# Optimization experiments

Measured on AMD Instinct MI355X. Metric: run time of the kernel, lower is better.

The kernel has to match this reference:

```python
import jax, jax.numpy as jnp
import numpy as np

B, T, IN, H, STEPS = 32768, 11, 2, 64, 80


def gru_cell(x, h, W_ih, W_hh, b_ih, b_hh):
    # PyTorch GRU cell: gates ordered (r, z, n)
    gi = x @ W_ih.T + b_ih            # [B, 3H]
    gh = h @ W_hh.T + b_hh            # [B, 3H]
    gi_r, gi_z, gi_n = jnp.split(gi, 3, axis=-1)
    gh_r, gh_z, gh_n = jnp.split(gh, 3, axis=-1)
    r = jax.nn.sigmoid(gi_r + gh_r)
    z = jax.nn.sigmoid(gi_z + gh_z)
    n = jnp.tanh(gi_n + r * gh_n)
    return (1.0 - z) * n + z * h


def setup_inputs() -> dict:
    key = jax.random.key(0)
    ks = jax.random.split(key, 20)
    s = 1.0 / np.sqrt(H)
    u = lambda k, shape: jax.random.uniform(k, shape, jnp.float32, -s, s)
    inp = {"x": jax.random.normal(ks[0], (B, T, IN), jnp.float32)}
    i = 1
    for pfx, in0 in (("e", IN), ("d", IN)):
        for l, d_in in ((0, in0), (1, H)):
            inp[f"{pfx}W_ih{l}"] = u(ks[i], (3 * H, d_in)); i += 1
            inp[f"{pfx}W_hh{l}"] = u(ks[i], (3 * H, H)); i += 1
            inp[f"{pfx}b_ih{l}"] = u(ks[i], (3 * H,)); i += 1
            inp[f"{pfx}b_hh{l}"] = u(ks[i], (3 * H,)); i += 1
    inp["fc_W"] = u(ks[17], (2, H))
    inp["fc_b"] = u(ks[18], (2,))
    return inp


def reference(x, eW_ih0, eW_hh0, eb_ih0, eb_hh0, eW_ih1, eW_hh1, eb_ih1, eb_hh1,
              dW_ih0, dW_hh0, db_ih0, db_hh0, dW_ih1, dW_hh1, db_ih1, db_hh1,
              fc_W, fc_b):
    b = x.shape[0]
    h0 = jnp.zeros((b, H), x.dtype)
    h1 = jnp.zeros((b, H), x.dtype)

    # ---- encoder: 2-layer GRU over time (dropout inactive in eval) ----
    def enc_step(carry, xt):
        c0, c1 = carry
        c0 = gru_cell(xt, c0, eW_ih0, eW_hh0, eb_ih0, eb_hh0)
        c1 = gru_cell(c0, c1, eW_ih1, eW_hh1, eb_ih1, eb_hh1)
        return (c0, c1), None

    (h0, h1), _ = jax.lax.scan(enc_step, (h0, h1), jnp.swapaxes(x, 0, 1))

    def dec_step(carry, _):
        inp, c0, c1 = carry
        c0 = gru_cell(inp, c0, dW_ih0, dW_hh0, db_ih0, db_hh0)
        c1 = gru_cell(c0, c1, dW_ih1, dW_hh1, db_ih1, db_hh1)
        pred = c1 @ fc_W.T + fc_b     # [B, 2]
        return (pred, c0, c1), pred

    init = (x[:, -1, :], h0, h1)
    _, preds = jax.lax.scan(dec_step, init, None, length=STEPS)  # [80, B, 2]
    return jnp.swapaxes(preds, 0, 1)  # [B, 80, 2]
```

## Files before the change

### kernel.cpp

```cpp
#include <hip/hip_runtime.h>
#include <cstddef>

#define T_SEQ 11
#define STEPS 80

typedef _Float16 f16;
typedef _Float16 f16x4 __attribute__((ext_vector_type(4)));
typedef _Float16 f16x8 __attribute__((ext_vector_type(8)));
typedef float    f32x4 __attribute__((ext_vector_type(4)));

#define SRC (-1.44269504f)
#define SNC ( 2.88539008f)

__device__ __forceinline__ f32x4 mfma16(f16x8 a, f16x8 b, f32x4 c) {
    return __builtin_amdgcn_mfma_f32_16x16x32_f16(a, b, c, 0, 0, 0);
}
__device__ __forceinline__ float exp2r(float x) { return __builtin_amdgcn_exp2f(x); }

__device__ __forceinline__ f16x8 wfrag(const float* __restrict__ W, int row, int k0, float sc) {
    f16x8 r;
    #pragma unroll
    for (int i = 0; i < 8; ++i) r[i] = (f16)(sc * W[row * 64 + k0 + i]);
    return r;
}
__device__ __forceinline__ f16x8 cfrag(const float* __restrict__ Wih0,
                                       const float* __restrict__ fcW, int row, int k0, float sc) {
    f16x8 r;
    #pragma unroll
    for (int i = 0; i < 8; ++i)
        r[i] = (f16)(sc * (Wih0[row * 2] * fcW[k0 + i] + Wih0[row * 2 + 1] * fcW[64 + k0 + i]));
    return r;
}

struct WSet {
    f16x8 xR[2], xZ[2], xN[2];
    f16x8 hR[2], hZ[2], hN[2];
};

__device__ __forceinline__ void load_h_frags(WSet& W, const float* __restrict__ Whh,
                                             int jA, int quad)
{
    #pragma unroll
    for (int ks = 0; ks < 2; ++ks) {
        const int k0 = ks * 32 + quad * 8;
        W.hR[ks] = wfrag(Whh, jA,       k0, SRC);
        W.hZ[ks] = wfrag(Whh, jA + 64,  k0, SRC);
        W.hN[ks] = wfrag(Whh, jA + 128, k0, SNC);
    }
}
__device__ __forceinline__ void load_x_frags(WSet& W, const float* __restrict__ Wx,
                                             int jA, int quad)
{
    #pragma unroll
    for (int ks = 0; ks < 2; ++ks) {
        const int k0 = ks * 32 + quad * 8;
        W.xR[ks] = wfrag(Wx, jA,       k0, SRC);
        W.xZ[ks] = wfrag(Wx, jA + 64,  k0, SRC);
        W.xN[ks] = wfrag(Wx, jA + 128, k0, SNC);
    }
}

template<bool XM, int CT>
__device__ __forceinline__ void cellH(const WSet& W, const float* __restrict__ sb,
    const f16* __restrict__ Xs, const f16* __restrict__ Hs, f16* __restrict__ Dst,
    f16x4& ho, const f32x4* __restrict__ xw, float2 xv,
    int j4, int ro0, int ro1, int wo)
{
    const f32x4 bR  = *(const f32x4*)(sb + CT * 256 +       j4);
    const f32x4 bZ  = *(const f32x4*)(sb + CT * 256 +  64 + j4);
    const f32x4 bNi = *(const f32x4*)(sb + CT * 256 + 128 + j4);
    const f32x4 bNh = *(const f32x4*)(sb + CT * 256 + 192 + j4);
    f16x8 hb0 = *(const f16x8*)(Hs + ro0);
    f16x8 hb1 = *(const f16x8*)(Hs + ro1);
    f32x4 aR  = mfma16(W.hR[0], hb0, bR);
    f32x4 aZ  = mfma16(W.hZ[0], hb0, bZ);
    f32x4 aNh = mfma16(W.hN[0], hb0, bNh);
    aR  = mfma16(W.hR[1], hb1, aR);
    aZ  = mfma16(W.hZ[1], hb1, aZ);
    aNh = mfma16(W.hN[1], hb1, aNh);
    f32x4 aNi;
    if constexpr (XM) {
        f16x8 xb0 = *(const f16x8*)(Xs + ro0);
        f16x8 xb1 = *(const f16x8*)(Xs + ro1);
        aR  = mfma16(W.xR[0], xb0, aR);    aR  = mfma16(W.xR[1], xb1, aR);
        aZ  = mfma16(W.xZ[0], xb0, aZ);    aZ  = mfma16(W.xZ[1], xb1, aZ);
        aNi = mfma16(W.xN[0], xb0, bNi);   aNi = mfma16(W.xN[1], xb1, aNi);
    } else {
        aR  += xv.x * xw[0] + xv.y * xw[1];
        aZ  += xv.x * xw[2] + xv.y * xw[3];
        aNi  = bNi + xv.x * xw[4] + xv.y * xw[5];
    }
    f16x4 o;
    #pragma unroll
    for (int i = 0; i < 4; ++i) {
        const float r = __builtin_amdgcn_rcpf(1.f + exp2r(aR[i]));
        const float z = __builtin_amdgcn_rcpf(1.f + exp2r(aZ[i]));
        const float n = 1.f - 2.f * __builtin_amdgcn_rcpf(1.f + exp2r(aNi[i] + r * aNh[i]));
        const float h = n + z * ((float)ho[i] - n);
        o[i] = (f16)h;
    }
    ho = o;
    *(f16x4*)(Dst + wo) = o;
}

__global__ __launch_bounds__(512, 4)
void gru_traj_pipe1(
    const float* __restrict__ x,
    const float* __restrict__ eWih0, const float* __restrict__ eWhh0,
    const float* __restrict__ ebih0, const float* __restrict__ ebhh0,
    const float* __restrict__ eWih1, const float* __restrict__ eWhh1,
    const float* __restrict__ ebih1, const float* __restrict__ ebhh1,
    const float* __restrict__ dWih0, const float* __restrict__ dWhh0,
    const float* __restrict__ dbih0, const float* __restrict__ dbhh0,
    const float* __restrict__ dWih1, const float* __restrict__ dWhh1,
    const float* __restrict__ dbih1, const float* __restrict__ dbhh1,
    const float* __restrict__ fcW,  const float* __restrict__ fcb,
    float* __restrict__ out)
{
    __shared__ f16 h0b[4][1024];
    __shared__ f16 h1b[4][1024];
    __shared__ float2 xe[T_SEQ * 32];
    __shared__ float sbias[4 * 256];
    __shared__ f16 sfc[1024];
    __shared__ float sfcb[2];

    const int tid  = threadIdx.x;
    const int lane = tid & 63;
    const int wv   = __builtin_amdgcn_readfirstlane(tid >> 6);
    const bool isL0 = wv < 4;
    const int jg   = wv & 3;
    const int quad = lane >> 4;
    const int col  = lane & 15;
    const int r0   = blockIdx.x * 32;

    {
        const float2* x2 = (const float2*)x;
        for (int i = tid; i < 32 * T_SEQ; i += 512) {
            const int row = i / T_SEQ, t = i - row * T_SEQ;
            xe[t * 32 + row] = x2[(size_t)r0 * T_SEQ + i];
        }
    }
    for (int i = tid; i < 2048; i += 512) {
        ((f16*)h0b)[i] = (f16)0.f; ((f16*)h1b)[i] = (f16)0.f;
    }
    if (tid < 64) {
        const int j = tid;
        sbias[       j] = SRC * (ebih0[j] + ebhh0[j]);
        sbias[ 64 + j] = SRC * (ebih0[64 + j] + ebhh0[64 + j]);
        sbias[128 + j] = SNC * ebih0[128 + j];
        sbias[192 + j] = SNC * ebhh0[128 + j];
        sbias[256 +       j] = SRC * (ebih1[j] + ebhh1[j]);
        sbias[256 +  64 + j] = SRC * (ebih1[64 + j] + ebhh1[64 + j]);
        sbias[256 + 128 + j] = SNC * ebih1[128 + j];
        sbias[256 + 192 + j] = SNC * ebhh1[128 + j];
    }
    for (int e = tid; e < 1024; e += 512) {
        const int ks = e >> 9, rr = e & 511;
        const int lne = rr >> 3, ki = rr & 7;
        const int c = lne & 15, q = lne >> 4;
        const int k = ks * 32 + q * 8 + ki;
        sfc[ks * 512 + lne * 8 + ki] = (c < 2) ? (f16)fcW[c * 64 + k] : (f16)0.f;
    }
    if (tid < 2) sfcb[tid] = fcb[tid];

    const int c7  = col & 7;
    const int ro0 = col * 64 + ((quad ^ c7) << 3);
    const int ro1 = col * 64 + (((4 + quad) ^ c7) << 3);
    const int wo  = col * 64 + ((((jg << 1) | (quad >> 1)) ^ c7) << 3) + ((quad & 1) << 2);
    const int jA  = jg * 16 + col;
    const int j4  = jg * 16 + quad * 4;

    f16x4 hoA, hoB;
    #pragma unroll
    for (int i = 0; i < 4; ++i) { hoA[i] = (f16)0.f; hoB[i] = (f16)0.f; }

    WSet W;
    f32x4 xw[6];
    if (isL0) {
        load_h_frags(W, eWhh0, jA, quad);
        #pragma unroll
        for (int rg = 0; rg < 4; ++rg) {
            xw[0][rg] = SRC * eWih0[(j4 + rg) * 2];        xw[1][rg] = SRC * eWih0[(j4 + rg) * 2 + 1];
            xw[2][rg] = SRC * eWih0[(64 + j4 + rg) * 2];   xw[3][rg] = SRC * eWih0[(64 + j4 + rg) * 2 + 1];
            xw[4][rg] = SNC * eWih0[(128 + j4 + rg) * 2];  xw[5][rg] = SNC * eWih0[(128 + j4 + rg) * 2 + 1];
        }
    } else {
        load_h_frags(W, eWhh1, jA, quad);
        load_x_frags(W, eWih1, jA, quad);
    }
    __syncthreads();

    #pragma unroll 1
    for (int t = 0; t < T_SEQ; ++t) {
        const int pr = t & 1, pw = pr ^ 1;
        if (isL0) {
            const float2 xv = xe[t * 32 + col];
            cellH<false, 0>(W, sbias, nullptr, h0b[pr * 2 + 0], h0b[pw * 2 + 0], hoA, xw, xv, j4, ro0, ro1, wo);
        } else if (t > 0) {
            cellH<true, 1>(W, sbias, h0b[pr * 2 + 1], h1b[pw * 2 + 1], h1b[pr * 2 + 1], hoB, xw, make_float2(0.f, 0.f), j4, ro0, ro1, wo);
        }
        __syncthreads();
        if (isL0) {
            const float2 xv = xe[t * 32 + 16 + col];
            cellH<false, 0>(W, sbias, nullptr, h0b[pr * 2 + 1], h0b[pw * 2 + 1], hoB, xw, xv, j4, ro0, ro1, wo);
        } else {
            cellH<true, 1>(W, sbias, h0b[pw * 2 + 0], h1b[pr * 2 + 0], h1b[pw * 2 + 0], hoA, xw, make_float2(0.f, 0.f), j4, ro0, ro1, wo);
        }
        __syncthreads();
    }
    if (!isL0)
        cellH<true, 1>(W, sbias, h0b[1 * 2 + 1], h1b[0 * 2 + 1], h1b[1 * 2 + 1], hoB, xw, make_float2(0.f, 0.f), j4, ro0, ro1, wo);
    __syncthreads();

    if (isL0) {
        load_h_frags(W, dWhh0, jA, quad);
        #pragma unroll
        for (int ks = 0; ks < 2; ++ks) {
            const int k0 = ks * 32 + quad * 8;
            W.xR[ks] = cfrag(dWih0, fcW, jA,       k0, SRC);
            W.xZ[ks] = cfrag(dWih0, fcW, jA + 64,  k0, SRC);
            W.xN[ks] = cfrag(dWih0, fcW, jA + 128, k0, SNC);
        }
        #pragma unroll
        for (int rg = 0; rg < 4; ++rg) {
            xw[0][rg] = SRC * dWih0[(j4 + rg) * 2];        xw[1][rg] = SRC * dWih0[(j4 + rg) * 2 + 1];
            xw[2][rg] = SRC * dWih0[(64 + j4 + rg) * 2];   xw[3][rg] = SRC * dWih0[(64 + j4 + rg) * 2 + 1];
            xw[4][rg] = SNC * dWih0[(128 + j4 + rg) * 2];  xw[5][rg] = SNC * dWih0[(128 + j4 + rg) * 2 + 1];
        }
    } else {
        load_h_frags(W, dWhh1, jA, quad);
        load_x_frags(W, dWih1, jA, quad);
    }
    if (tid < 64) {
        const int j = tid;
        const float f0 = fcb[0], f1 = fcb[1];
        sbias[512 +       j] = SRC * (dbih0[j] + dbhh0[j] + dWih0[j * 2] * f0 + dWih0[j * 2 + 1] * f1);
        sbias[512 +  64 + j] = SRC * (dbih0[64 + j] + dbhh0[64 + j] + dWih0[(64 + j) * 2] * f0 + dWih0[(64 + j) * 2 + 1] * f1);
        sbias[512 + 128 + j] = SNC * (dbih0[128 + j] + dWih0[(128 + j) * 2] * f0 + dWih0[(128 + j) * 2 + 1] * f1);
        sbias[512 + 192 + j] = SNC * dbhh0[128 + j];
        sbias[768 +       j] = SRC * (dbih1[j] + dbhh1[j]);
        sbias[768 +  64 + j] = SRC * (dbih1[64 + j] + dbhh1[64 + j]);
        sbias[768 + 128 + j] = SNC * dbih1[128 + j];
        sbias[768 + 192 + j] = SNC * dbhh1[128 + j];
    }
    __syncthreads();

    float* op = out + (size_t)(r0 + jg * 16 + col) * (STEPS * 2);
    auto FCOUT = [&](const f16* __restrict__ h1c) {
        f32x4 pb;
        pb[0] = (quad == 0) ? sfcb[0] : 0.f;
        pb[1] = (quad == 0) ? sfcb[1] : 0.f;
        pb[2] = 0.f; pb[3] = 0.f;
        f16x8 fc0 = *(const f16x8*)(sfc + lane * 8);
        f16x8 fc1 = *(const f16x8*)(sfc + 512 + lane * 8);
        f16x8 hb0 = *(const f16x8*)(h1c + ro0);
        f16x8 hb1 = *(const f16x8*)(h1c + ro1);
        f32x4 p = mfma16(fc0, hb0, pb);
        p = mfma16(fc1, hb1, p);
        if (quad == 0) *(float2*)op = make_float2(p[0], p[1]);
        op += 2;
    };

    if (isL0) {
        const float2 xv = xe[10 * 32 + col];
        cellH<false, 2>(W, sbias, nullptr, h0b[1 * 2 + 0], h0b[0 * 2 + 0], hoA, xw, xv, j4, ro0, ro1, wo);
    }
    __syncthreads();
    if (isL0) {
        const float2 xv = xe[10 * 32 + 16 + col];
        cellH<false, 2>(W, sbias, nullptr, h0b[1 * 2 + 1], h0b[0 * 2 + 1], hoB, xw, xv, j4, ro0, ro1, wo);
    } else {
        cellH<true, 3>(W, sbias, h0b[0 * 2 + 0], h1b[1 * 2 + 0], h1b[0 * 2 + 0], hoA, xw, make_float2(0.f, 0.f), j4, ro0, ro1, wo);
    }
    __syncthreads();

    #pragma unroll 1
    for (int s = 1; s < STEPS; ++s) {
        const int pr = s & 1, pw = pr ^ 1;
        if (isL0) {
            cellH<true, 2>(W, sbias, h1b[pw * 2 + 0], h0b[pw * 2 + 0], h0b[pr * 2 + 0], hoA, xw, make_float2(0.f, 0.f), j4, ro0, ro1, wo);
        } else {
            cellH<true, 3>(W, sbias, h0b[pw * 2 + 1], h1b[pr * 2 + 1], h1b[pw * 2 + 1], hoB, xw, make_float2(0.f, 0.f), j4, ro0, ro1, wo);
            if (jg == 0) FCOUT(h1b[pw * 2 + 0]);
        }
        __syncthreads();
        if (isL0) {
            cellH<true, 2>(W, sbias, h1b[pw * 2 + 1], h0b[pw * 2 + 1], h0b[pr * 2 + 1], hoB, xw, make_float2(0.f, 0.f), j4, ro0, ro1, wo);
        } else {
            cellH<true, 3>(W, sbias, h0b[pr * 2 + 0], h1b[pw * 2 + 0], h1b[pr * 2 + 0], hoA, xw, make_float2(0.f, 0.f), j4, ro0, ro1, wo);
            if (jg == 1) FCOUT(h1b[pw * 2 + 1]);
        }
        __syncthreads();
    }
    if (!isL0) {
        cellH<true, 3>(W, sbias, h0b[1 * 2 + 1], h1b[0 * 2 + 1], h1b[1 * 2 + 1], hoB, xw, make_float2(0.f, 0.f), j4, ro0, ro1, wo);
        if (jg == 0) FCOUT(h1b[1 * 2 + 0]);
    }
    __syncthreads();
    if (!isL0 && jg == 1) FCOUT(h1b[1 * 2 + 1]);
}

extern "C" void kernel_launch(void* const* d_in, const int* in_sizes, int n_in,
                              void* d_out, int out_size, void* d_ws, size_t ws_size,
                              hipStream_t stream) {
    (void)n_in; (void)out_size; (void)d_ws; (void)ws_size;

    const float* x     = (const float*)d_in[0];
    const float* eWih0 = (const float*)d_in[1];
    const float* eWhh0 = (const float*)d_in[2];
    const float* ebih0 = (const float*)d_in[3];
    const float* ebhh0 = (const float*)d_in[4];
    const float* eWih1 = (const float*)d_in[5];
    const float* eWhh1 = (const float*)d_in[6];
    const float* ebih1 = (const float*)d_in[7];
    const float* ebhh1 = (const float*)d_in[8];
    const float* dWih0 = (const float*)d_in[9];
    const float* dWhh0 = (const float*)d_in[10];
    const float* dbih0 = (const float*)d_in[11];
    const float* dbhh0 = (const float*)d_in[12];
    const float* dWih1 = (const float*)d_in[13];
    const float* dWhh1 = (const float*)d_in[14];
    const float* dbih1 = (const float*)d_in[15];
    const float* dbhh1 = (const float*)d_in[16];
    const float* fcW   = (const float*)d_in[17];
    const float* fcb   = (const float*)d_in[18];
    float* out = (float*)d_out;

    const int b = in_sizes[0] / (T_SEQ * 2);
    dim3 grid(b / 32), block(512);
    hipLaunchKernelGGL(gru_traj_pipe1, grid, block, 0, stream,
        x, eWih0, eWhh0, ebih0, ebhh0, eWih1, eWhh1, ebih1, ebhh1,
        dWih0, dWhh0, dbih0, dbhh0, dWih1, dWhh1, dbih1, dbhh1,
        fcW, fcb, out);
}
```

Baseline: 470.0 us.

## Switch GRU kernel to 32x32x16 MFMA tiles with bias folded into MFMA

Replaces the 16x16x32 MFMA cell with a 32x32x16 variant. Each block now handles 64 batch rows with 4 waves instead of 32 rows with 8 waves, so each wave owns a 32-unit half of the hidden dimension. Biases and the 2-wide layer-0 input projection are folded into an extra MFMA by packing weights and a split hi/lo bias into spare K slots, which removes the shared bias table and the scalar FMA path. Wave roles alternate by block parity to balance which SIMD hosts layer 0. This cuts per-wave instruction overhead, but it raises register pressure (larger weight fragments and accumulators) and lowers the wave count per block.

Measured after the change: 485.7 us. 3.3% more time.

```diff
diff --git a/kernel.cpp b/kernel.cpp
--- a/kernel.cpp
+++ b/kernel.cpp
@@ -8,103 +8,87 @@
 typedef _Float16 f16x4 __attribute__((ext_vector_type(4)));
 typedef _Float16 f16x8 __attribute__((ext_vector_type(8)));
 typedef float    f32x4 __attribute__((ext_vector_type(4)));
+typedef float    f32x16 __attribute__((ext_vector_type(16)));
 
 #define SRC (-1.44269504f)
 #define SNC ( 2.88539008f)
 
-__device__ __forceinline__ f32x4 mfma16(f16x8 a, f16x8 b, f32x4 c) {
-    return __builtin_amdgcn_mfma_f32_16x16x32_f16(a, b, c, 0, 0, 0);
+__device__ __forceinline__ f32x16 mfma32(f16x8 a, f16x8 b, f32x16 c) {
+    return __builtin_amdgcn_mfma_f32_32x32x16_f16(a, b, c, 0, 0, 0);
 }
 __device__ __forceinline__ float exp2r(float x) { return __builtin_amdgcn_exp2f(x); }
 
-__device__ __forceinline__ f16x8 wfrag(const float* __restrict__ W, int row, int k0, float sc) {
+__device__ __forceinline__ f16x8 afrag32(const float* __restrict__ W, int rowBase,
+                                         int b31, int hi, int f, float sc) {
     f16x8 r;
+    const int row = rowBase + b31, k0 = f * 16 + hi * 8;
     #pragma unroll
     for (int i = 0; i < 8; ++i) r[i] = (f16)(sc * W[row * 64 + k0 + i]);
     return r;
 }
-__device__ __forceinline__ f16x8 cfrag(const float* __restrict__ Wih0,
-                                       const float* __restrict__ fcW, int row, int k0, float sc) {
+__device__ __forceinline__ f16x8 cfrag32(const float* __restrict__ Wih0,
+                                         const float* __restrict__ fcW, int rowBase,
+                                         int b31, int hi, int f, float sc) {
     f16x8 r;
+    const int row = rowBase + b31, k0 = f * 16 + hi * 8;
     #pragma unroll
     for (int i = 0; i < 8; ++i)
         r[i] = (f16)(sc * (Wih0[row * 2] * fcW[k0 + i] + Wih0[row * 2 + 1] * fcW[64 + k0 + i]));
     return r;
 }
-
-struct WSet {
-    f16x8 xR[2], xZ[2], xN[2];
-    f16x8 hR[2], hZ[2], hN[2];
-};
-
-__device__ __forceinline__ void load_h_frags(WSet& W, const float* __restrict__ Whh,
-                                             int jA, int quad)
+__device__ __forceinline__ f16x8 ex_make(float w0, float w1, float b, int hi) {
+    f16x8 r;
+    #pragma unroll
+    for (int i = 0; i < 8; ++i) r[i] = (f16)0.f;
+    if (hi == 0) {
+        r[0] = (f16)w0; r[1] = (f16)w1;
+        const float bh = (float)(f16)b;
+        r[6] = (f16)bh; r[7] = (f16)(256.f * (b - bh));
+    }
+    return r;
+}
+
+template<bool XM>
+__device__ __forceinline__ void cell32(
+    const f16x8 (&Wh)[3][4], const f16x8 (&Wx)[3][4], const f16x8 (&ex)[4], f16x8 exB,
+    const f16* __restrict__ Xs, const f16* __restrict__ Hs, f16* __restrict__ Dst,
+    f16x4 (&ho)[4], const int (&rd)[4], const int (&wr)[4])
 {
-    #pragma unroll
-    for (int ks = 0; ks < 2; ++ks) {
-        const int k0 = ks * 32 + quad * 8;
-        W.hR[ks] = wfrag(Whh, jA,       k0, SRC);
-        W.hZ[ks] = wfrag(Whh, jA + 64,  k0, SRC);
-        W.hN[ks] = wfrag(Whh, jA + 128, k0, SNC);
-    }
-}
-__device__ __forceinline__ void load_x_frags(WSet& W, const float* __restrict__ Wx,
-                                             int jA, int quad)
-{
-    #pragma unroll
-    for (int ks = 0; ks < 2; ++ks) {
-        const int k0 = ks * 32 + quad * 8;
-        W.xR[ks] = wfrag(Wx, jA,       k0, SRC);
-        W.xZ[ks] = wfrag(Wx, jA + 64,  k0, SRC);
-        W.xN[ks] = wfrag(Wx, jA + 128, k0, SNC);
-    }
-}
-
-template<bool XM, int CT>
-__device__ __forceinline__ void cellH(const WSet& W, const float* __restrict__ sb,
-    const f16* __restrict__ Xs, const f16* __restrict__ Hs, f16* __restrict__ Dst,
-    f16x4& ho, const f32x4* __restrict__ xw, float2 xv,
-    int j4, int ro0, int ro1, int wo)
-{
-    const f32x4 bR  = *(const f32x4*)(sb + CT * 256 +       j4);
-    const f32x4 bZ  = *(const f32x4*)(sb + CT * 256 +  64 + j4);
-    const f32x4 bNi = *(const f32x4*)(sb + CT * 256 + 128 + j4);
-    const f32x4 bNh = *(const f32x4*)(sb + CT * 256 + 192 + j4);
-    f16x8 hb0 = *(const f16x8*)(Hs + ro0);
-    f16x8 hb1 = *(const f16x8*)(Hs + ro1);
-    f32x4 aR  = mfma16(W.hR[0], hb0, bR);
-    f32x4 aZ  = mfma16(W.hZ[0], hb0, bZ);
-    f32x4 aNh = mfma16(W.hN[0], hb0, bNh);
-    aR  = mfma16(W.hR[1], hb1, aR);
-    aZ  = mfma16(W.hZ[1], hb1, aZ);
-    aNh = mfma16(W.hN[1], hb1, aNh);
-    f32x4 aNi;
-    if constexpr (XM) {
-        f16x8 xb0 = *(const f16x8*)(Xs + ro0);
-        f16x8 xb1 = *(const f16x8*)(Xs + ro1);
-        aR  = mfma16(W.xR[0], xb0, aR);    aR  = mfma16(W.xR[1], xb1, aR);
-        aZ  = mfma16(W.xZ[0], xb0, aZ);    aZ  = mfma16(W.xZ[1], xb1, aZ);
-        aNi = mfma16(W.xN[0], xb0, bNi);   aNi = mfma16(W.xN[1], xb1, aNi);
-    } else {
-        aR  += xv.x * xw[0] + xv.y * xw[1];
-        aZ  += xv.x * xw[2] + xv.y * xw[3];
-        aNi  = bNi + xv.x * xw[4] + xv.y * xw[5];
-    }
-    f16x4 o;
-    #pragma unroll
-    for (int i = 0; i < 4; ++i) {
-        const float r = __builtin_amdgcn_rcpf(1.f + exp2r(aR[i]));
-        const float z = __builtin_amdgcn_rcpf(1.f + exp2r(aZ[i]));
-        const float n = 1.f - 2.f * __builtin_amdgcn_rcpf(1.f + exp2r(aNi[i] + r * aNh[i]));
-        const float h = n + z * ((float)ho[i] - n);
-        o[i] = (f16)h;
-    }
-    ho = o;
-    *(f16x4*)(Dst + wo) = o;
-}
-
-__global__ __launch_bounds__(512, 4)
-void gru_traj_pipe1(
+    f32x16 z;
+    #pragma unroll
+    for (int i = 0; i < 16; ++i) z[i] = 0.f;
+    f32x16 aR  = mfma32(ex[0], exB, z);
+    f32x16 aZ  = mfma32(ex[1], exB, z);
+    f32x16 aNi = mfma32(ex[2], exB, z);
+    f32x16 aNh = mfma32(ex[3], exB, z);
+    #pragma unroll
+    for (int f = 0; f < 4; ++f) {
+        const f16x8 hb = *(const f16x8*)(Hs + rd[f]);
+        aR  = mfma32(Wh[0][f], hb, aR);
+        aZ  = mfma32(Wh[1][f], hb, aZ);
+        aNh = mfma32(Wh[2][f], hb, aNh);
+        if constexpr (XM) {
+            const f16x8 xb = *(const f16x8*)(Xs + rd[f]);
+            aR  = mfma32(Wx[0][f], xb, aR);
+            aZ  = mfma32(Wx[1][f], xb, aZ);
+            aNi = mfma32(Wx[2][f], xb, aNi);
+        }
+    }
+    f16x4 o[4];
+    #pragma unroll
+    for (int r = 0; r < 16; ++r) {
+        const float rr = __builtin_amdgcn_rcpf(1.f + exp2r(aR[r]));
+        const float zz = __builtin_amdgcn_rcpf(1.f + exp2r(aZ[r]));
+        const float n  = 1.f - 2.f * __builtin_amdgcn_rcpf(1.f + exp2r(aNi[r] + rr * aNh[r]));
+        const float h  = n + zz * ((float)ho[r >> 2][r & 3] - n);
+        o[r >> 2][r & 3] = (f16)h;
+    }
+    #pragma unroll
+    for (int g = 0; g < 4; ++g) { ho[g] = o[g]; *(f16x4*)(Dst + wr[g]) = o[g]; }
+}
+
+__global__ __launch_bounds__(256, 2)
+void gru_traj_w32(
     const float* __restrict__ x,
     const float* __restrict__ eWih0, const float* __restrict__ eWhh0,
     const float* __restrict__ ebih0, const float* __restrict__ ebhh0,
@@ -117,76 +101,83 @@
     const float* __restrict__ fcW,  const float* __restrict__ fcb,
     float* __restrict__ out)
 {
-    __shared__ f16 h0b[4][1024];
-    __shared__ f16 h1b[4][1024];
-    __shared__ float2 xe[T_SEQ * 32];
-    __shared__ float sbias[4 * 256];
-    __shared__ f16 sfc[1024];
-    __shared__ float sfcb[2];
+    __shared__ f16 h0s[2 * 2 * 2048];
+    __shared__ f16 h1s[2 * 2 * 2048];
+    __shared__ float2 xs[T_SEQ * 64];
+#define H0(p, hf) (h0s + ((p) * 2 + (hf)) * 2048)
+#define H1(p, hf) (h1s + ((p) * 2 + (hf)) * 2048)
 
     const int tid  = threadIdx.x;
     const int lane = tid & 63;
     const int wv   = __builtin_amdgcn_readfirstlane(tid >> 6);
-    const bool isL0 = wv < 4;
-    const int jg   = wv & 3;
-    const int quad = lane >> 4;
-    const int col  = lane & 15;
-    const int r0   = blockIdx.x * 32;
+    const int wvr  = (wv + ((blockIdx.x & 1) << 1)) & 3;
+    const bool isL0 = wvr < 2;
+    const int jh   = wvr & 1;
+    const int b31  = lane & 31;
+    const int hi   = lane >> 5;
+    const int b7   = b31 & 7;
+    const int r0   = blockIdx.x * 64;
 
     {
         const float2* x2 = (const float2*)x;
-        for (int i = tid; i < 32 * T_SEQ; i += 512) {
+        for (int i = tid; i < 64 * T_SEQ; i += 256) {
             const int row = i / T_SEQ, t = i - row * T_SEQ;
-            xe[t * 32 + row] = x2[(size_t)r0 * T_SEQ + i];
-        }
-    }
-    for (int i = tid; i < 2048; i += 512) {
-        ((f16*)h0b)[i] = (f16)0.f; ((f16*)h1b)[i] = (f16)0.f;
-    }
-    if (tid < 64) {
-        const int j = tid;
-        sbias[       j] = SRC * (ebih0[j] + ebhh0[j]);
-        sbias[ 64 + j] = SRC * (ebih0[64 + j] + ebhh0[64 + j]);
-        sbias[128 + j] = SNC * ebih0[128 + j];
-        sbias[192 + j] = SNC * ebhh0[128 + j];
-        sbias[256 +       j] = SRC * (ebih1[j] + ebhh1[j]);
-        sbias[256 +  64 + j] = SRC * (ebih1[64 + j] + ebhh1[64 + j]);
-        sbias[256 + 128 + j] = SNC * ebih1[128 + j];
-        sbias[256 + 192 + j] = SNC * ebhh1[128 + j];
-    }
-    for (int e = tid; e < 1024; e += 512) {
-        const int ks = e >> 9, rr = e & 511;
-        const int lne = rr >> 3, ki = rr & 7;
-        const int c = lne & 15, q = lne >> 4;
-        const int k = ks * 32 + q * 8 + ki;
-        sfc[ks * 512 + lne * 8 + ki] = (c < 2) ? (f16)fcW[c * 64 + k] : (f16)0.f;
-    }
-    if (tid < 2) sfcb[tid] = fcb[tid];
-
-    const int c7  = col & 7;
-    const int ro0 = col * 64 + ((quad ^ c7) << 3);
-    const int ro1 = col * 64 + (((4 + quad) ^ c7) << 3);
-    const int wo  = col * 64 + ((((jg << 1) | (quad >> 1)) ^ c7) << 3) + ((quad & 1) << 2);
-    const int jA  = jg * 16 + col;
-    const int j4  = jg * 16 + quad * 4;
-
-    f16x4 hoA, hoB;
-    #pragma unroll
-    for (int i = 0; i < 4; ++i) { hoA[i] = (f16)0.f; hoB[i] = (f16)0.f; }
-
-    WSet W;
-    f32x4 xw[6];
+            xs[t * 64 + row] = x2[(size_t)r0 * T_SEQ + i];
+        }
+    }
+    for (int i = tid; i < 4096; i += 256) { h0s[i] = (f16)0.f; h1s[i] = (f16)0.f; }
+
+    int rd[4], wr[4];
+    #pragma unroll
+    for (int f = 0; f < 4; ++f) rd[f] = b31 * 64 + (((f * 2 + hi) ^ b7) << 3);
+    #pragma unroll
+    for (int g = 0; g < 4; ++g) wr[g] = b31 * 64 + ((((jh << 2) + g) ^ b7) << 3) + (hi << 2);
+
+    const int jA = jh * 32 + b31;
+
+    f16x8 exB1;
+    #pragma unroll
+    for (int i = 0; i < 8; ++i) exB1[i] = (f16)0.f;
+    if (hi == 0) { exB1[6] = (f16)1.f; exB1[7] = (f16)(1.f / 256.f); }
+    auto exBx = [&](float2 xv) {
+        f16x8 r;
+        #pragma unroll
+        for (int i = 0; i < 8; ++i) r[i] = (f16)0.f;
+        if (hi == 0) { r[0] = (f16)xv.x; r[1] = (f16)xv.y; r[6] = (f16)1.f; r[7] = (f16)(1.f / 256.f); }
+        return r;
+    };
+
+    f16x4 hoA[4], hoB[4];
+    #pragma unroll
+    for (int g = 0; g < 4; ++g) {
+        #pragma unroll
+        for (int i = 0; i < 4; ++i) { hoA[g][i] = (f16)0.f; hoB[g][i] = (f16)0.f; }
+    }
+
+    f16x8 Wh[3][4], Wx[3][4], ex[4];
     if (isL0) {
-        load_h_frags(W, eWhh0, jA, quad);
-        #pragma unroll
-        for (int rg = 0; rg < 4; ++rg) {
-            xw[0][rg] = SRC * eWih0[(j4 + rg) * 2];        xw[1][rg] = SRC * eWih0[(j4 + rg) * 2 + 1];
-            xw[2][rg] = SRC * eWih0[(64 + j4 + rg) * 2];   xw[3][rg] = SRC * eWih0[(64 + j4 + rg) * 2 + 1];
-            xw[4][rg] = SNC * eWih0[(128 + j4 + rg) * 2];  xw[5][rg] = SNC * eWih0[(128 + j4 + rg) * 2 + 1];
-        }
+        #pragma unroll
+        for (int g = 0; g < 3; ++g)
+            #pragma unroll
+            for (int f = 0; f < 4; ++f)
+                Wh[g][f] = afrag32(eWhh0, g * 64 + jh * 32, b31, hi, f, g == 2 ? SNC : SRC);
+        ex[0] = ex_make(SRC * eWih0[jA * 2],         SRC * eWih0[jA * 2 + 1],         SRC * (ebih0[jA] + ebhh0[jA]), hi);
+        ex[1] = ex_make(SRC * eWih0[(64 + jA) * 2],  SRC * eWih0[(64 + jA) * 2 + 1],  SRC * (ebih0[64 + jA] + ebhh0[64 + jA]), hi);
+        ex[2] = ex_make(SNC * eWih0[(128 + jA) * 2], SNC * eWih0[(128 + jA) * 2 + 1], SNC * ebih0[128 + jA], hi);
+        ex[3] = ex_make(0.f, 0.f, SNC * ebhh0[128 + jA], hi);
     } else {
-        load_h_frags(W, eWhh1, jA, quad);
-        load_x_frags(W, eWih1, jA, quad);
+        #pragma unroll
+        for (int g = 0; g < 3; ++g)
+            #pragma unroll
+            for (int f = 0; f < 4; ++f) {
+                const float sc = g == 2 ? SNC : SRC;
+                Wh[g][f] = afrag32(eWhh1, g * 64 + jh * 32, b31, hi, f, sc);
+                Wx[g][f] = afrag32(eWih1, g * 64 + jh * 32, b31, hi, f, sc);
+            }
+        ex[0] = ex_make(0.f, 0.f, SRC * (ebih1[jA] + ebhh1[jA]), hi);
+        ex[1] = ex_make(0.f, 0.f, SRC * (ebih1[64 + jA] + ebhh1[64 + jA]), hi);
+        ex[2] = ex_make(0.f, 0.f, SNC * ebih1[128 + jA], hi);
+        ex[3] = ex_make(0.f, 0.f, SNC * ebhh1[128 + jA], hi);
     }
     __syncthreads();
 
@@ -194,110 +185,128 @@
     for (int t = 0; t < T_SEQ; ++t) {
         const int pr = t & 1, pw = pr ^ 1;
         if (isL0) {
-            const float2 xv = xe[t * 32 + col];
-            cellH<false, 0>(W, sbias, nullptr, h0b[pr * 2 + 0], h0b[pw * 2 + 0], hoA, xw, xv, j4, ro0, ro1, wo);
+            cell32<false>(Wh, Wh, ex, exBx(xs[t * 64 + b31]),
+                          nullptr, H0(pr, 0), H0(pw, 0), hoA, rd, wr);
         } else if (t > 0) {
-            cellH<true, 1>(W, sbias, h0b[pr * 2 + 1], h1b[pw * 2 + 1], h1b[pr * 2 + 1], hoB, xw, make_float2(0.f, 0.f), j4, ro0, ro1, wo);
+            cell32<true>(Wh, Wx, ex, exB1, H0(pr, 1), H1(pw, 1), H1(pr, 1), hoB, rd, wr);
         }
         __syncthreads();
         if (isL0) {
-            const float2 xv = xe[t * 32 + 16 + col];
-            cellH<false, 0>(W, sbias, nullptr, h0b[pr * 2 + 1], h0b[pw * 2 + 1], hoB, xw, xv, j4, ro0, ro1, wo);
+            cell32<false>(Wh, Wh, ex, exBx(xs[t * 64 + 32 + b31]),
+                          nullptr, H0(pr, 1), H0(pw, 1), hoB, rd, wr);
         } else {
-            cellH<true, 1>(W, sbias, h0b[pw * 2 + 0], h1b[pr * 2 + 0], h1b[pw * 2 + 0], hoA, xw, make_float2(0.f, 0.f), j4, ro0, ro1, wo);
+            cell32<true>(Wh, Wx, ex, exB1, H0(pw, 0), H1(pr, 0), H1(pw, 0), hoA, rd, wr);
         }
         __syncthreads();
     }
     if (!isL0)
-        cellH<true, 1>(W, sbias, h0b[1 * 2 + 1], h1b[0 * 2 + 1], h1b[1 * 2 + 1], hoB, xw, make_float2(0.f, 0.f), j4, ro0, ro1, wo);
-    __syncthreads();
-
+        cell32<true>(Wh, Wx, ex, exB1, H0(1, 1), H1(0, 1), H1(1, 1), hoB, rd, wr);
+    __syncthreads();
+
+    f16x8 fcA[4];
+    float fcb0 = fcb[0], fcb1 = fcb[1];
     if (isL0) {
-        load_h_frags(W, dWhh0, jA, quad);
-        #pragma unroll
-        for (int ks = 0; ks < 2; ++ks) {
-            const int k0 = ks * 32 + quad * 8;
-            W.xR[ks] = cfrag(dWih0, fcW, jA,       k0, SRC);
-            W.xZ[ks] = cfrag(dWih0, fcW, jA + 64,  k0, SRC);
-            W.xN[ks] = cfrag(dWih0, fcW, jA + 128, k0, SNC);
-        }
-        #pragma unroll
-        for (int rg = 0; rg < 4; ++rg) {
-            xw[0][rg] = SRC * dWih0[(j4 + rg) * 2];        xw[1][rg] = SRC * dWih0[(j4 + rg) * 2 + 1];
-            xw[2][rg] = SRC * dWih0[(64 + j4 + rg) * 2];   xw[3][rg] = SRC * dWih0[(64 + j4 + rg) * 2 + 1];
-            xw[4][rg] = SNC * dWih0[(128 + j4 + rg) * 2];  xw[5][rg] = SNC * dWih0[(128 + j4 + rg) * 2 + 1];
-        }
+        #pragma unroll
+        for (int g = 0; g < 3; ++g)
+            #pragma unroll
+            for (int f = 0; f < 4; ++f)
+                Wh[g][f] = afrag32(dWhh0, g * 64 + jh * 32, b31, hi, f, g == 2 ? SNC : SRC);
+        ex[0] = ex_make(SRC * dWih0[jA * 2],         SRC * dWih0[jA * 2 + 1],         SRC * (dbih0[jA] + dbhh0[jA]), hi);
+        ex[1] = ex_make(SRC * dWih0[(64 + jA) * 2],  SRC * dWih0[(64 + jA) * 2 + 1],  SRC * (dbih0[64 + jA] + dbhh0[64 + jA]), hi);
+        ex[2] = ex_make(SNC * dWih0[(128 + jA) * 2], SNC * dWih0[(128 + jA) * 2 + 1], SNC * dbih0[128 + jA], hi);
+        ex[3] = ex_make(0.f, 0.f, SNC * dbhh0[128 + jA], hi);
     } else {
-        load_h_frags(W, dWhh1, jA, quad);
-        load_x_frags(W, dWih1, jA, quad);
-    }
-    if (tid < 64) {
-        const int j = tid;
-        const float f0 = fcb[0], f1 = fcb[1];
-        sbias[512 +       j] = SRC * (dbih0[j] + dbhh0[j] + dWih0[j * 2] * f0 + dWih0[j * 2 + 1] * f1);
-        sbias[512 +  64 + j] = SRC * (dbih0[64 + j] + dbhh0[64 + j] + dWih0[(64 + j) * 2] * f0 + dWih0[(64 + j) * 2 + 1] * f1);
-        sbias[512 + 128 + j] = SNC * (dbih0[128 + j] + dWih0[(128 + j) * 2] * f0 + dWih0[(128 + j) * 2 + 1] * f1);
-        sbias[512 + 192 + j] = SNC * dbhh0[128 + j];
-        sbias[768 +       j] = SRC * (dbih1[j] + dbhh1[j]);
-        sbias[768 +  64 + j] = SRC * (dbih1[64 + j] + dbhh1[64 + j]);
-        sbias[768 + 128 + j] = SNC * dbih1[128 + j];
-        sbias[768 + 192 + j] = SNC * dbhh1[128 + j];
-    }
-    __syncthreads();
-
-    float* op = out + (size_t)(r0 + jg * 16 + col) * (STEPS * 2);
+        #pragma unroll
+        for (int g = 0; g < 3; ++g)
+            #pragma unroll
+            for (int f = 0; f < 4; ++f) {
+                const float sc = g == 2 ? SNC : SRC;
+                Wh[g][f] = afrag32(dWhh1, g * 64 + jh * 32, b31, hi, f, sc);
+                Wx[g][f] = afrag32(dWih1, g * 64 + jh * 32, b31, hi, f, sc);
+            }
+        ex[0] = ex_make(0.f, 0.f, SRC * (dbih1[jA] + dbhh1[jA]), hi);
+        ex[1] = ex_make(0.f, 0.f, SRC * (dbih1[64 + jA] + dbhh1[64 + jA]), hi);
+        ex[2] = ex_make(0.f, 0.f, SNC * dbih1[128 + jA], hi);
+        ex[3] = ex_make(0.f, 0.f, SNC * dbhh1[128 + jA], hi);
+        #pragma unroll
+        for (int f = 0; f < 4; ++f) {
+            f16x8 r;
+            #pragma unroll
+            for (int i = 0; i < 8; ++i) r[i] = (f16)0.f;
+            if (b31 < 2) {
+                const int k0 = f * 16 + hi * 8;
+                #pragma unroll
+                for (int i = 0; i < 8; ++i) r[i] = (f16)fcW[b31 * 64 + k0 + i];
+            }
+            fcA[f] = r;
+        }
+    }
+
+    float* op = out + (size_t)(r0 + jh * 32 + b31) * (STEPS * 2);
     auto FCOUT = [&](const f16* __restrict__ h1c) {
-        f32x4 pb;
-        pb[0] = (quad == 0) ? sfcb[0] : 0.f;
-        pb[1] = (quad == 0) ? sfcb[1] : 0.f;
-        pb[2] = 0.f; pb[3] = 0.f;
-        f16x8 fc0 = *(const f16x8*)(sfc + lane * 8);
-        f16x8 fc1 = *(const f16x8*)(sfc + 512 + lane * 8);
-        f16x8 hb0 = *(const f16x8*)(h1c + ro0);
-        f16x8 hb1 = *(const f16x8*)(h1c + ro1);
-        f32x4 p = mfma16(fc0, hb0, pb);
-        p = mfma16(fc1, hb1, p);
-        if (quad == 0) *(float2*)op = make_float2(p[0], p[1]);
+        f32x16 pc;
+        #pragma unroll
+        for (int i = 0; i < 16; ++i) pc[i] = 0.f;
+        if (hi == 0) { pc[0] = fcb0; pc[1] = fcb1; }
+        #pragma unroll
+        for (int f = 0; f < 4; ++f) {
+            const f16x8 hb = *(const f16x8*)(h1c + rd[f]);
+            pc = mfma32(fcA[f], hb, pc);
+        }
+        if (hi == 0) *(float2*)op = make_float2(pc[0], pc[1]);
         op += 2;
     };
 
+    if (isL0)
+        cell32<false>(Wh, Wh, ex, exBx(xs[10 * 64 + b31]),
+                      nullptr, H0(1, 0), H0(0, 0), hoA, rd, wr);
+    __syncthreads();
     if (isL0) {
-        const float2 xv = xe[10 * 32 + col];
-        cellH<false, 2>(W, sbias, nullptr, h0b[1 * 2 + 0], h0b[0 * 2 + 0], hoA, xw, xv, j4, ro0, ro1, wo);
-    }
-    __syncthreads();
+        cell32<false>(Wh, Wh, ex, exBx(xs[10 * 64 + 32 + b31]),
+                      nullptr, H0(1, 1), H0(0, 1), hoB, rd, wr);
+    } else {
+        cell32<true>(Wh, Wx, ex, exB1, H0(0, 0), H1(1, 0), H1(0, 0), hoA, rd, wr);
+    }
+    __syncthreads();
+
     if (isL0) {
-        const float2 xv = xe[10 * 32 + 16 + col];
-        cellH<false, 2>(W, sbias, nullptr, h0b[1 * 2 + 1], h0b[0 * 2 + 1], hoB, xw, xv, j4, ro0, ro1, wo);
-    } else {
-        cellH<true, 3>(W, sbias, h0b[0 * 2 + 0], h1b[1 * 2 + 0], h1b[0 * 2 + 0], hoA, xw, make_float2(0.f, 0.f), j4, ro0, ro1, wo);
-    }
-    __syncthreads();
+        #pragma unroll
+        for (int g = 0; g < 3; ++g)
+            #pragma unroll
+            for (int f = 0; f < 4; ++f)
+                Wx[g][f] = cfrag32(dWih0, fcW, g * 64 + jh * 32, b31, hi, f, g == 2 ? SNC : SRC);
+        ex[0] = ex_make(0.f, 0.f, SRC * (dbih0[jA] + dbhh0[jA] + dWih0[jA * 2] * fcb0 + dWih0[jA * 2 + 1] * fcb1), hi);
+        ex[1] = ex_make(0.f, 0.f, SRC * (dbih0[64 + jA] + dbhh0[64 + jA] + dWih0[(64 + jA) * 2] * fcb0 + dWih0[(64 + jA) * 2 + 1] * fcb1), hi);
+        ex[2] = ex_make(0.f, 0.f, SNC * (dbih0[128 + jA] + dWih0[(128 + jA) * 2] * fcb0 + dWih0[(128 + jA) * 2 + 1] * fcb1), hi);
+        ex[3] = ex_make(0.f, 0.f, SNC * dbhh0[128 + jA], hi);
+    }
 
     #pragma unroll 1
     for (int s = 1; s < STEPS; ++s) {
         const int pr = s & 1, pw = pr ^ 1;
         if (isL0) {
-            cellH<true, 2>(W, sbias, h1b[pw * 2 + 0], h0b[pw * 2 + 0], h0b[pr * 2 + 0], hoA, xw, make_float2(0.f, 0.f), j4, ro0, ro1, wo);
+            cell32<true>(Wh, Wx, ex, exB1, H1(pw, 0), H0(pw, 0), H0(pr, 0), hoA, rd, wr);
         } else {
-            cellH<true, 3>(W, sbias, h0b[pw * 2 + 1], h1b[pr * 2 + 1], h1b[pw * 2 + 1], hoB, xw, make_float2(0.f, 0.f), j4, ro0, ro1, wo);
-            if (jg == 0) FCOUT(h1b[pw * 2 + 0]);
+            cell32<true>(Wh, Wx, ex, exB1, H0(pw, 1), H1(pr, 1), H1(pw, 1), hoB, rd, wr);
+            if (jh == 0) FCOUT(H1(pw, 0));
         }
         __syncthreads();
         if (isL0) {
-            cellH<true, 2>(W, sbias, h1b[pw * 2 + 1], h0b[pw * 2 + 1], h0b[pr * 2 + 1], hoB, xw, make_float2(0.f, 0.f), j4, ro0, ro1, wo);
+            cell32<true>(Wh, Wx, ex, exB1, H1(pw, 1), H0(pw, 1), H0(pr, 1), hoB, rd, wr);
         } else {
-            cellH<true, 3>(W, sbias, h0b[pr * 2 + 0], h1b[pw * 2 + 0], h1b[pr * 2 + 0], hoA, xw, make_float2(0.f, 0.f), j4, ro0, ro1, wo);
-            if (jg == 1) FCOUT(h1b[pw * 2 + 1]);
+            cell32<true>(Wh, Wx, ex, exB1, H0(pr, 0), H1(pw, 0), H1(pr, 0), hoA, rd, wr);
+            if (jh == 1) FCOUT(H1(pw, 1));
         }
         __syncthreads();
     }
     if (!isL0) {
-        cellH<true, 3>(W, sbias, h0b[1 * 2 + 1], h1b[0 * 2 + 1], h1b[1 * 2 + 1], hoB, xw, make_float2(0.f, 0.f), j4, ro0, ro1, wo);
-        if (jg == 0) FCOUT(h1b[1 * 2 + 0]);
-    }
-    __syncthreads();
-    if (!isL0 && jg == 1) FCOUT(h1b[1 * 2 + 1]);
+        cell32<true>(Wh, Wx, ex, exB1, H0(1, 1), H1(0, 1), H1(1, 1), hoB, rd, wr);
+        if (jh == 0) FCOUT(H1(1, 0));
+    }
+    __syncthreads();
+    if (!isL0 && jh == 1) FCOUT(H1(1, 1));
+#undef H0
+#undef H1
 }
 
 extern "C" void kernel_launch(void* const* d_in, const int* in_sizes, int n_in,
@@ -327,8 +336,8 @@
     float* out = (float*)d_out;
 
     const int b = in_sizes[0] / (T_SEQ * 2);
-    dim3 grid(b / 32), block(512);
-    hipLaunchKernelGGL(gru_traj_pipe1, grid, block, 0, stream,
+    dim3 grid(b / 64), block(256);
+    hipLaunchKernelGGL(gru_traj_w32, grid, block, 0, stream,
         x, eWih0, eWhh0, ebih0, ebhh0, eWih1, eWhh1, ebih1, ebhh1,
         dWih0, dWhh0, dbih0, dbhh0, dWih1, dWhh1, dbih1, dbhh1,
         fcW, fcb, out);
```
